# Kernel optimization log

Measured on AMD Instinct MI355X. Metric: run time of the kernel, lower is better.

The kernel has to match this reference:

```python
import jax, jax.numpy as jnp
import numpy as np

DELTA_PULL = 0.5
DELTA_PUSH = 1.5
EPS = 1e-6


def setup_inputs() -> dict:
    key = jax.random.key(0)
    k1, k2 = jax.random.split(key)
    B, C, H, W, K = 4, 16, 512, 512, 16
    embedding_maps = jax.random.normal(k1, (B, C, H, W), dtype=jnp.float32)
    instance_masks = jax.random.randint(k2, (B, K, H, W), 0, 2, dtype=jnp.int32)
    return {"embedding_maps": embedding_maps, "instance_masks": instance_masks}


def reference(embedding_maps, instance_masks):
    emb = embedding_maps                      # [B, C, H, W]
    m = (instance_masks > 0).astype(emb.dtype)  # [B, K, H, W]
    K = m.shape[1]

    # per-instance masked segment reductions over all H*W pixels
    counts = m.sum((-1, -2))                                   # [B, K]
    sums = jnp.einsum('bchw,bkhw->bkc', emb, m)                # [B, K, C]
    sq_sums = jnp.einsum('bchw,bkhw->bkc', emb * emb, m)       # [B, K, C]

    valid = counts > 0                                          # [B, K]
    safe_counts = jnp.maximum(counts, 1.0)
    means = sums / safe_counts[..., None]                       # [B, K, C] exact fg mean

    # sum over fg pixels of ||e - mean||^2 = sq_sum - 2*mean.sum + n*mean^2
    pull_k = (sq_sums - 2.0 * means * sums + counts[..., None] * means * means).sum(-1)
    pull_k = jnp.where(valid, pull_k / (counts + EPS), 0.0)     # [B, K]

    M = valid.sum(-1).astype(emb.dtype)                         # [B] num valid instances
    pull_b = pull_k.sum(-1) / jnp.maximum(M, 1.0)               # [B]

    # pairwise push between valid instance means (i < j)
    diff = means[:, :, None, :] - means[:, None, :, :]          # [B, K, K, C]
    dist = jnp.sqrt((diff * diff).sum(-1) + 1e-12)              # [B, K, K]
    iu = jnp.arange(K)
    pair = valid[:, :, None] & valid[:, None, :] & (iu[:, None] < iu[None, :])
    push_terms = jnp.where(pair, jnp.maximum(DELTA_PUSH - dist, 0.0) ** 2, 0.0)
    npairs = M * (M - 1.0) / 2.0
    push_b = jnp.where(M > 1.0, push_terms.sum((-1, -2)) / jnp.maximum(npairs, 1.0), 0.0)

    return (DELTA_PULL * pull_b + push_b).mean()
```

## Files before the change

### kernel.cpp

```cpp
#include <hip/hip_runtime.h>

#define BB 4
#define CC 16
#define KK 16
#define HWP (512 * 512)
#define TPB 512
#define TPW 128
#define NTILES (HWP / TPB)
#define THREADS 256
#define NSLICE 32
#define WSTOT (64 + 1024 + 1024)

typedef short bf16x8 __attribute__((ext_vector_type(8)));
typedef float f32x4 __attribute__((ext_vector_type(4)));

__device__ __forceinline__ float fmaxf_(float a, float b) { return a > b ? a : b; }

__device__ __forceinline__ unsigned short f2bf(float f) {
    unsigned u = __float_as_uint(f);
    u += 0x7FFFu + ((u >> 16) & 1u);
    return (unsigned short)(u >> 16);
}
__device__ __forceinline__ unsigned pkbf(float x, float y) {
    return (unsigned)f2bf(x) | ((unsigned)f2bf(y) << 16);
}
__device__ __forceinline__ unsigned pkmask(int a, int b) {
    unsigned ua = (a > 0) ? 1u : 0u;
    unsigned ub = (b > 0) ? 1u : 0u;
    return (ua | (ub << 16)) * 0x3F80u;
}

__global__ __launch_bounds__(THREADS) void disc_mfma_kernel(
    const float* __restrict__ emb, const int* __restrict__ masks,
    float* __restrict__ ws)
{
    const int tid = threadIdx.x;
    const int lane = tid & 63;
    const int wave = tid >> 6;
    const int b = blockIdx.x / NTILES;
    const int tile = blockIdx.x % NTILES;
    const size_t base_px = (size_t)tile * TPB + wave * TPW;

    const int quad = lane >> 4;
    const int r = lane & 15;

    const int*   mplane = masks + ((size_t)b * KK + r) * HWP + base_px + quad * 8;
    const float* eplane = emb   + ((size_t)b * CC + r) * HWP + base_px + quad * 8;

    int4 m0[4], m1[4]; float4 e0[4], e1[4];
    #pragma unroll
    for (int g = 0; g < 4; ++g) {
        const int4* mp = (const int4*)(mplane + g * 32);
        m0[g] = mp[0]; m1[g] = mp[1];
        const float4* ep = (const float4*)(eplane + g * 32);
        e0[g] = ep[0]; e1[g] = ep[1];
    }

    union { bf16x8 v; unsigned short s[8]; } Bones;
    #pragma unroll
    for (int i = 0; i < 8; ++i) Bones.s[i] = 0x3F80;

    f32x4 acc_s = {0.f, 0.f, 0.f, 0.f};
    f32x4 acc_q = {0.f, 0.f, 0.f, 0.f};
    f32x4 acc_c = {0.f, 0.f, 0.f, 0.f};

    #pragma unroll
    for (int g = 0; g < 4; ++g) {
        union { bf16x8 v; unsigned u[4]; } A;
        A.u[0] = pkmask(m0[g].x, m0[g].y);
        A.u[1] = pkmask(m0[g].z, m0[g].w);
        A.u[2] = pkmask(m1[g].x, m1[g].y);
        A.u[3] = pkmask(m1[g].z, m1[g].w);

        union { bf16x8 v; unsigned u[4]; } Bf, B2;
        Bf.u[0] = pkbf(e0[g].x, e0[g].y);
        Bf.u[1] = pkbf(e0[g].z, e0[g].w);
        Bf.u[2] = pkbf(e1[g].x, e1[g].y);
        Bf.u[3] = pkbf(e1[g].z, e1[g].w);
        B2.u[0] = pkbf(e0[g].x * e0[g].x, e0[g].y * e0[g].y);
        B2.u[1] = pkbf(e0[g].z * e0[g].z, e0[g].w * e0[g].w);
        B2.u[2] = pkbf(e1[g].x * e1[g].x, e1[g].y * e1[g].y);
        B2.u[3] = pkbf(e1[g].z * e1[g].z, e1[g].w * e1[g].w);

        acc_s = __builtin_amdgcn_mfma_f32_16x16x32_bf16(A.v, Bf.v, acc_s, 0, 0, 0);
        acc_q = __builtin_amdgcn_mfma_f32_16x16x32_bf16(A.v, B2.v, acc_q, 0, 0, 0);
        acc_c = __builtin_amdgcn_mfma_f32_16x16x32_bf16(A.v, Bones.v, acc_c, 0, 0, 0);
    }

    float* slice = ws + (size_t)((blockIdx.x * 4 + wave) & (NSLICE - 1)) * WSTOT;
    #pragma unroll
    for (int reg = 0; reg < 4; ++reg) {
        const int krow = quad * 4 + reg;
        atomicAdd(&slice[64 + ((size_t)b * KK + krow) * CC + r], acc_s[reg]);
        atomicAdd(&slice[64 + 1024 + ((size_t)b * KK + krow) * CC + r], acc_q[reg]);
    }
    if (r == 0) {
        #pragma unroll
        for (int reg = 0; reg < 4; ++reg) {
            atomicAdd(&slice[b * KK + quad * 4 + reg], acc_c[reg]);
        }
    }
}

__global__ __launch_bounds__(256) void disc_finalize_kernel(
    const float* __restrict__ ws, float* __restrict__ out)
{
    __shared__ float red[WSTOT];
    __shared__ float means[BB][KK][CC];
    __shared__ float partial[BB];
    const int tid = threadIdx.x;

    for (int idx = tid; idx < WSTOT; idx += 256) {
        float t = 0.f;
        #pragma unroll
        for (int s = 0; s < NSLICE; ++s) t += ws[(size_t)s * WSTOT + idx];
        red[idx] = t;
    }
    __syncthreads();

    const float* red_cnt = red;
    const float* red_sum = red + 64;
    const float* red_sq  = red + 64 + 1024;

    const int b = tid >> 6;
    const int lane = tid & 63;

    const float DELTA_PULL = 0.5f;
    const float DELTA_PUSH = 1.5f;
    const float EPS = 1e-6f;

    float cntk = 0.f;
    bool valid = false;
    float pull_k = 0.f;
    if (lane < KK) {
        int k = lane;
        cntk = red_cnt[b * KK + k];
        valid = cntk > 0.f;
        float safe = fmaxf_(cntk, 1.f);
        float acc_sq = 0.f, acc_ss = 0.f;
        #pragma unroll
        for (int c = 0; c < CC; ++c) {
            float sv = red_sum[(b * KK + k) * CC + c];
            means[b][k][c] = sv / safe;
            acc_sq += red_sq[(b * KK + k) * CC + c];
            acc_ss += sv * sv;
        }
        if (valid) pull_k = (acc_sq - acc_ss / cntk) / (cntk + EPS);
    }

    unsigned long long bal = __ballot(lane < KK && valid);
    float M = (float)__popcll(bal);

    float ps = pull_k;
    #pragma unroll
    for (int d = 32; d >= 1; d >>= 1) ps += __shfl_xor(ps, d, 64);
    float pull_b = ps / fmaxf_(M, 1.f);

    __syncthreads();

    float push = 0.f;
    for (int t = lane; t < KK * KK; t += 64) {
        int i = t >> 4, j = t & 15;
        if (i < j && ((bal >> i) & 1ull) && ((bal >> j) & 1ull)) {
            float d2 = 1e-12f;
            #pragma unroll
            for (int c = 0; c < CC; ++c) {
                float df = means[b][i][c] - means[b][j][c];
                d2 = fmaf(df, df, d2);
            }
            float dist = sqrtf(d2);
            float h = fmaxf_(DELTA_PUSH - dist, 0.f);
            push += h * h;
        }
    }
    #pragma unroll
    for (int d = 32; d >= 1; d >>= 1) push += __shfl_xor(push, d, 64);

    if (lane == 0) {
        float npairs = M * (M - 1.f) * 0.5f;
        float push_b = (M > 1.f) ? push / fmaxf_(npairs, 1.f) : 0.f;
        partial[b] = DELTA_PULL * pull_b + push_b;
    }
    __syncthreads();
    if (tid == 0) {
        out[0] = (partial[0] + partial[1] + partial[2] + partial[3]) * 0.25f;
    }
}

extern "C" void kernel_launch(void* const* d_in, const int* in_sizes, int n_in,
                              void* d_out, int out_size, void* d_ws, size_t ws_size,
                              hipStream_t stream) {
    const float* emb = (const float*)d_in[0];
    const int* masks = (const int*)d_in[1];
    float* ws = (float*)d_ws;

    hipMemsetAsync(d_ws, 0, NSLICE * WSTOT * sizeof(float), stream);

    dim3 grid(BB * NTILES);
    disc_mfma_kernel<<<grid, THREADS, 0, stream>>>(emb, masks, ws);
    disc_finalize_kernel<<<1, 256, 0, stream>>>(ws, (float*)d_out);
}
```

Measured before the change: 170.9 us.

## Double per-block tile, prefetch next group, reduce waves in LDS before atomics

Each block now covers twice as many pixels, with eight 32-pixel groups per wave. The next group's mask and embedding loads are issued before the current group is converted and fed to MFMA, with a sched barrier to keep them apart. Per-wave accumulators are summed across the four waves in shared memory, so each block issues one set of global atomics instead of four, and the slice count is halved. The aim is fewer atomics and better latency hiding. The cost is fewer blocks in flight and an extra __syncthreads.

```diff
diff --git a/kernel.cpp b/kernel.cpp
--- a/kernel.cpp
+++ b/kernel.cpp
@@ -4,11 +4,12 @@
 #define CC 16
 #define KK 16
 #define HWP (512 * 512)
-#define TPB 512
-#define TPW 128
+#define TPB 1024
+#define TPW 256
 #define NTILES (HWP / TPB)
 #define THREADS 256
-#define NSLICE 32
+#define NGROUP (TPW / 32)
+#define NSLICE 16
 #define WSTOT (64 + 1024 + 1024)
 
 typedef short bf16x8 __attribute__((ext_vector_type(8)));
@@ -34,6 +35,9 @@
     const float* __restrict__ emb, const int* __restrict__ masks,
     float* __restrict__ ws)
 {
+    __shared__ float redbuf[4][64][9];
+    __shared__ float cnt_red[4][16];
+
     const int tid = threadIdx.x;
     const int lane = tid & 63;
     const int wave = tid >> 6;
@@ -44,17 +48,8 @@
     const int quad = lane >> 4;
     const int r = lane & 15;
 
-    const int*   mplane = masks + ((size_t)b * KK + r) * HWP + base_px + quad * 8;
-    const float* eplane = emb   + ((size_t)b * CC + r) * HWP + base_px + quad * 8;
-
-    int4 m0[4], m1[4]; float4 e0[4], e1[4];
-    #pragma unroll
-    for (int g = 0; g < 4; ++g) {
-        const int4* mp = (const int4*)(mplane + g * 32);
-        m0[g] = mp[0]; m1[g] = mp[1];
-        const float4* ep = (const float4*)(eplane + g * 32);
-        e0[g] = ep[0]; e1[g] = ep[1];
-    }
+    const int*   mp = masks + ((size_t)b * KK + r) * HWP + base_px + quad * 8;
+    const float* ep = emb   + ((size_t)b * CC + r) * HWP + base_px + quad * 8;
 
     union { bf16x8 v; unsigned short s[8]; } Bones;
     #pragma unroll
@@ -64,41 +59,70 @@
     f32x4 acc_q = {0.f, 0.f, 0.f, 0.f};
     f32x4 acc_c = {0.f, 0.f, 0.f, 0.f};
 
-    #pragma unroll
-    for (int g = 0; g < 4; ++g) {
+    int4 m0c = ((const int4*)mp)[0], m1c = ((const int4*)mp)[1];
+    float4 e0c = ((const float4*)ep)[0], e1c = ((const float4*)ep)[1];
+
+    #pragma unroll
+    for (int g = 0; g < NGROUP; ++g) {
+        int4 m0n, m1n; float4 e0n, e1n;
+        if (g + 1 < NGROUP) {
+            const int*   mpn = mp + (g + 1) * 32;
+            const float* epn = ep + (g + 1) * 32;
+            m0n = ((const int4*)mpn)[0]; m1n = ((const int4*)mpn)[1];
+            e0n = ((const float4*)epn)[0]; e1n = ((const float4*)epn)[1];
+        }
+#if __has_builtin(__builtin_amdgcn_sched_barrier)
+        __builtin_amdgcn_sched_barrier(0);
+#endif
         union { bf16x8 v; unsigned u[4]; } A;
-        A.u[0] = pkmask(m0[g].x, m0[g].y);
-        A.u[1] = pkmask(m0[g].z, m0[g].w);
-        A.u[2] = pkmask(m1[g].x, m1[g].y);
-        A.u[3] = pkmask(m1[g].z, m1[g].w);
+        A.u[0] = pkmask(m0c.x, m0c.y);
+        A.u[1] = pkmask(m0c.z, m0c.w);
+        A.u[2] = pkmask(m1c.x, m1c.y);
+        A.u[3] = pkmask(m1c.z, m1c.w);
 
         union { bf16x8 v; unsigned u[4]; } Bf, B2;
-        Bf.u[0] = pkbf(e0[g].x, e0[g].y);
-        Bf.u[1] = pkbf(e0[g].z, e0[g].w);
-        Bf.u[2] = pkbf(e1[g].x, e1[g].y);
-        Bf.u[3] = pkbf(e1[g].z, e1[g].w);
-        B2.u[0] = pkbf(e0[g].x * e0[g].x, e0[g].y * e0[g].y);
-        B2.u[1] = pkbf(e0[g].z * e0[g].z, e0[g].w * e0[g].w);
-        B2.u[2] = pkbf(e1[g].x * e1[g].x, e1[g].y * e1[g].y);
-        B2.u[3] = pkbf(e1[g].z * e1[g].z, e1[g].w * e1[g].w);
+        Bf.u[0] = pkbf(e0c.x, e0c.y);
+        Bf.u[1] = pkbf(e0c.z, e0c.w);
+        Bf.u[2] = pkbf(e1c.x, e1c.y);
+        Bf.u[3] = pkbf(e1c.z, e1c.w);
+        B2.u[0] = pkbf(e0c.x * e0c.x, e0c.y * e0c.y);
+        B2.u[1] = pkbf(e0c.z * e0c.z, e0c.w * e0c.w);
+        B2.u[2] = pkbf(e1c.x * e1c.x, e1c.y * e1c.y);
+        B2.u[3] = pkbf(e1c.z * e1c.z, e1c.w * e1c.w);
 
         acc_s = __builtin_amdgcn_mfma_f32_16x16x32_bf16(A.v, Bf.v, acc_s, 0, 0, 0);
         acc_q = __builtin_amdgcn_mfma_f32_16x16x32_bf16(A.v, B2.v, acc_q, 0, 0, 0);
         acc_c = __builtin_amdgcn_mfma_f32_16x16x32_bf16(A.v, Bones.v, acc_c, 0, 0, 0);
-    }
-
-    float* slice = ws + (size_t)((blockIdx.x * 4 + wave) & (NSLICE - 1)) * WSTOT;
-    #pragma unroll
-    for (int reg = 0; reg < 4; ++reg) {
-        const int krow = quad * 4 + reg;
-        atomicAdd(&slice[64 + ((size_t)b * KK + krow) * CC + r], acc_s[reg]);
-        atomicAdd(&slice[64 + 1024 + ((size_t)b * KK + krow) * CC + r], acc_q[reg]);
+
+        if (g + 1 < NGROUP) { m0c = m0n; m1c = m1n; e0c = e0n; e1c = e1n; }
+    }
+
+    #pragma unroll
+    for (int j = 0; j < 4; ++j) {
+        redbuf[wave][lane][j] = acc_s[j];
+        redbuf[wave][lane][4 + j] = acc_q[j];
     }
     if (r == 0) {
         #pragma unroll
-        for (int reg = 0; reg < 4; ++reg) {
-            atomicAdd(&slice[b * KK + quad * 4 + reg], acc_c[reg]);
-        }
+        for (int reg = 0; reg < 4; ++reg) cnt_red[wave][quad * 4 + reg] = acc_c[reg];
+    }
+    __syncthreads();
+
+    float* slice = ws + (size_t)(blockIdx.x & (NSLICE - 1)) * WSTOT;
+    #pragma unroll
+    for (int t = 0; t < 2; ++t) {
+        const int fi = tid + t * THREADS;
+        const int l2 = fi >> 3, j = fi & 7;
+        float v = redbuf[0][l2][j] + redbuf[1][l2][j]
+                + redbuf[2][l2][j] + redbuf[3][l2][j];
+        const int reg = j & 3, isq = j >> 2;
+        const int krow = (l2 >> 4) * 4 + reg;
+        const int ccol = l2 & 15;
+        atomicAdd(&slice[64 + isq * 1024 + ((size_t)b * KK + krow) * CC + ccol], v);
+    }
+    if (tid < KK) {
+        float ctot = cnt_red[0][tid] + cnt_red[1][tid] + cnt_red[2][tid] + cnt_red[3][tid];
+        atomicAdd(&slice[b * KK + tid], ctot);
     }
 }
 
```

Measured after the change: 158.7 us. -7.1%, faster.
